# Kernel optimization log

Measured on AMD Instinct MI355X. Metric: run time of the kernel, lower is better.

## Reference

```python
import jax, jax.numpy as jnp
import numpy as np

B, H, W, C = 4, 64, 64, 256
D = C // 8  # reduction_ratio = 8


def setup_inputs() -> dict:
    key = jax.random.key(0)
    ks = jax.random.split(key, 6)
    scale = 1.0 / np.sqrt(C)
    return {
        "x": jax.random.normal(ks[0], (B, H, W, C), dtype=jnp.float32),
        "Wf": jax.random.normal(ks[1], (C, D), dtype=jnp.float32) * scale,
        "Wg": jax.random.normal(ks[2], (C, D), dtype=jnp.float32) * scale,
        "Wh": jax.random.normal(ks[3], (C, D), dtype=jnp.float32) * scale,
        "Wv": jax.random.normal(ks[4], (D, C), dtype=jnp.float32) * (1.0 / np.sqrt(D)),
        "gamma": jax.random.normal(ks[5], (), dtype=jnp.float32),
    }


def reference(x, Wf, Wg, Wh, Wv, gamma):
    b, h, w, c = x.shape
    n = h * w
    xf = x.reshape(b, n, c)
    # 1x1 convs (no bias) == per-pixel matmuls over channels
    q = xf @ Wf  # [b, n, d]
    k = xf @ Wg  # [b, n, d]
    v = xf @ Wh  # [b, n, d]
    # beta[i, j] = k_i . q_j ; softmax over last (query) axis, unscaled
    beta = jax.nn.softmax(jnp.einsum('bnd,bmd->bnm', k, q), axis=-1)  # [b, n, n]
    o = jnp.einsum('bnm,bmd->bnd', beta, v)  # [b, n, d]
    o = o.reshape(b, h, w, -1) @ Wv  # output 1x1 conv -> [b, h, w, c]
    return gamma * o + x
```

## Files before the change

kernel.cpp:

```cpp
#include <hip/hip_runtime.h>
#include <hip/hip_bf16.h>
#include <stdint.h>


typedef __attribute__((ext_vector_type(8))) short bf16x8;
typedef __attribute__((ext_vector_type(4))) float f32x4;
typedef unsigned short ushort_t;

static __device__ __forceinline__ ushort_t f2bf(float f) {
    __hip_bfloat16 h = __float2bfloat16(f);
    return __builtin_bit_cast(ushort_t, h);
}
static __device__ __forceinline__ float bf2f(ushort_t u) {
    return __bfloat162float(__builtin_bit_cast(__hip_bfloat16, u));
}

#define NROWS 16384
#define NTOK  4096
#define QKS   40
#define PVS   72

__global__ __launch_bounds__(256) void prep_kernel(
    const float* __restrict__ Wf, const float* __restrict__ Wg,
    const float* __restrict__ Wh,
    ushort_t* __restrict__ WhT, ushort_t* __restrict__ WlT,
    float* __restrict__ zero_base)
{
    int bid = blockIdx.x;
    if (bid < 96) {
        int id  = bid * 256 + threadIdx.x;
        int a   = id >> 13, rem = id & 8191;
        int k   = rem >> 5, d = rem & 31;
        const float* Wsrc = (a == 0) ? Wf : (a == 1) ? Wg : Wh;
        float val = Wsrc[rem];
        ushort_t hi = f2bf(val);
        WhT[(a * 32 + d) * 256 + k] = hi;
        WlT[(a * 32 + d) * 256 + k] = f2bf(val - bf2f(hi));
    } else {
        int i = (bid - 96) * 1024 + threadIdx.x * 4;
        *reinterpret_cast<float4*>(&zero_base[i]) = (float4){0.f, 0.f, 0.f, 0.f};
    }
}

__global__ __launch_bounds__(256) void qkv_kernel(
    const float* __restrict__ x,
    const ushort_t* __restrict__ WhT, const ushort_t* __restrict__ WlT,
    ushort_t* __restrict__ qh,
    ushort_t* __restrict__ kh, ushort_t* __restrict__ kl,
    ushort_t* __restrict__ vh)
{
    __shared__ __align__(16) ushort_t xh[64 * QKS];
    __shared__ __align__(16) ushort_t xl[64 * QKS];

    const int tid  = threadIdx.x;
    const int wave = tid >> 6;
    const int lane = tid & 63;
    const int ln15 = lane & 15;
    const int quad = lane >> 4;
    const int row0 = blockIdx.x * 64;
    const int r    = tid >> 2;
    const int pp   = (tid & 3) * 8;

    f32x4 acc[6];
    #pragma unroll
    for (int s = 0; s < 6; ++s) acc[s] = (f32x4){0.f, 0.f, 0.f, 0.f};

    float4 xa = *reinterpret_cast<const float4*>(&x[(row0 + r) * 256 + pp]);
    float4 xb = *reinterpret_cast<const float4*>(&x[(row0 + r) * 256 + pp + 4]);

    for (int k0 = 0; k0 < 256; k0 += 32) {
        bf16x8 bh[6], bl[6];
        #pragma unroll
        for (int s = 0; s < 6; ++s) {
            bh[s] = *reinterpret_cast<const bf16x8*>(
                &WhT[(s * 16 + ln15) * 256 + k0 + quad * 8]);
            bl[s] = *reinterpret_cast<const bf16x8*>(
                &WlT[(s * 16 + ln15) * 256 + k0 + quad * 8]);
        }
        float fv[8];
        *reinterpret_cast<float4*>(&fv[0]) = xa;
        *reinterpret_cast<float4*>(&fv[4]) = xb;
        ushort_t hv[8], lv[8];
        #pragma unroll
        for (int j = 0; j < 8; ++j) {
            hv[j] = f2bf(fv[j]);
            lv[j] = f2bf(fv[j] - bf2f(hv[j]));
        }
        __syncthreads();
        *reinterpret_cast<uint4*>(&xh[r * QKS + pp]) = *reinterpret_cast<uint4*>(hv);
        *reinterpret_cast<uint4*>(&xl[r * QKS + pp]) = *reinterpret_cast<uint4*>(lv);
        __syncthreads();
        if (k0 < 224) {
            xa = *reinterpret_cast<const float4*>(&x[(row0 + r) * 256 + k0 + 32 + pp]);
            xb = *reinterpret_cast<const float4*>(&x[(row0 + r) * 256 + k0 + 36 + pp]);
        }
        const bf16x8 ah = *reinterpret_cast<const bf16x8*>(
            &xh[(wave * 16 + ln15) * QKS + quad * 8]);
        const bf16x8 al = *reinterpret_cast<const bf16x8*>(
            &xl[(wave * 16 + ln15) * QKS + quad * 8]);
        #pragma unroll
        for (int s = 0; s < 6; ++s) {
            acc[s] = __builtin_amdgcn_mfma_f32_16x16x32_bf16(ah, bh[s], acc[s], 0, 0, 0);
            acc[s] = __builtin_amdgcn_mfma_f32_16x16x32_bf16(al, bh[s], acc[s], 0, 0, 0);
            acc[s] = __builtin_amdgcn_mfma_f32_16x16x32_bf16(ah, bl[s], acc[s], 0, 0, 0);
        }
    }

    #pragma unroll
    for (int s = 0; s < 6; ++s) {
        int cc = (s & 1) * 16 + ln15;
        #pragma unroll
        for (int rr = 0; rr < 4; ++rr) {
            int row = row0 + wave * 16 + quad * 4 + rr;
            float val = acc[s][rr];
            ushort_t hi = f2bf(val);
            if (s < 2) {
                qh[row * 32 + cc] = hi;
            } else if (s < 4) {
                kh[row * 32 + cc] = hi;
                kl[row * 32 + cc] = f2bf(val - bf2f(hi));
            } else {
                vh[row * 32 + cc] = hi;
            }
        }
    }
}

__global__ __launch_bounds__(256, 4) void attn_kernel(
    const ushort_t* __restrict__ qhg,
    const ushort_t* __restrict__ khg, const ushort_t* __restrict__ klg,
    const ushort_t* __restrict__ vhg,
    float* __restrict__ o_num, float* __restrict__ l_glob)
{
    __shared__ __align__(16) ushort_t Khs[64 * QKS];
    __shared__ __align__(16) ushort_t Kls[64 * QKS];
    __shared__ __align__(16) ushort_t Qhs[2][64 * QKS];
    __shared__ __align__(16) ushort_t Vth[2][32 * PVS];
    __shared__ __align__(16) ushort_t Ps[4 * 16 * PVS];

    const int tid  = threadIdx.x;
    const int wave = tid >> 6;
    const int lane = tid & 63;
    const int ln15 = lane & 15;
    const int quad = lane >> 4;

    const int rowtile = blockIdx.x & 255;
    const int chunk   = blockIdx.x >> 8;
    const int b    = rowtile >> 6;
    const int n0   = (rowtile & 63) * 64;
    const int base = b * NTOK;
    const int mt0  = chunk * 16;

    const int r = tid >> 2;
    const int p = (tid & 3) * 8;

    {
        uint4 a0 = *reinterpret_cast<const uint4*>(&khg[(base + n0 + r) * 32 + p]);
        *reinterpret_cast<uint4*>(&Khs[r * QKS + p]) = a0;
        uint4 a1 = *reinterpret_cast<const uint4*>(&klg[(base + n0 + r) * 32 + p]);
        *reinterpret_cast<uint4*>(&Kls[r * QKS + p]) = a1;
    }
    {
        int m0 = mt0 * 64;
        uint4 t0 = *reinterpret_cast<const uint4*>(&qhg[(base + m0 + r) * 32 + p]);
        *reinterpret_cast<uint4*>(&Qhs[0][r * QKS + p]) = t0;
        uint4 v0 = *reinterpret_cast<const uint4*>(&vhg[(base + m0 + r) * 32 + p]);
        const ushort_t* vs = reinterpret_cast<const ushort_t*>(&v0);
        #pragma unroll
        for (int j = 0; j < 8; ++j)
            Vth[0][(p + j) * PVS + r] = vs[j];
    }
    __syncthreads();

    const bf16x8 khf = *reinterpret_cast<const bf16x8*>(
        &Khs[(wave * 16 + ln15) * QKS + quad * 8]);
    const bf16x8 klf = *reinterpret_cast<const bf16x8*>(
        &Kls[(wave * 16 + ln15) * QKS + quad * 8]);

    f32x4 accO[2];
    accO[0] = (f32x4){0.f, 0.f, 0.f, 0.f};
    accO[1] = (f32x4){0.f, 0.f, 0.f, 0.f};
    float lacc[4] = {0.f, 0.f, 0.f, 0.f};

    int buf = 0;
    for (int it = 0; it < 16; ++it) {
        uint4 nqh, nvh;
        if (it < 15) {
            int m1 = (mt0 + it + 1) * 64;
            nqh = *reinterpret_cast<const uint4*>(&qhg[(base + m1 + r) * 32 + p]);
            nvh = *reinterpret_cast<const uint4*>(&vhg[(base + m1 + r) * 32 + p]);
        }

        f32x4 st[4];
        #pragma unroll
        for (int t = 0; t < 4; ++t) {
            const bf16x8 qf = *reinterpret_cast<const bf16x8*>(
                &Qhs[buf][(t * 16 + ln15) * QKS + quad * 8]);
            f32x4 s = __builtin_amdgcn_mfma_f32_16x16x32_bf16(
                khf, qf, (f32x4){0.f, 0.f, 0.f, 0.f}, 0, 0, 0);
            s = __builtin_amdgcn_mfma_f32_16x16x32_bf16(klf, qf, s, 0, 0, 0);
            st[t] = s;
        }

        #pragma unroll
        for (int t = 0; t < 4; ++t)
            #pragma unroll
            for (int rr = 0; rr < 4; ++rr)
                st[t][rr] = __expf(st[t][rr]);
        #pragma unroll
        for (int rr = 0; rr < 4; ++rr)
            lacc[rr] += st[0][rr] + st[1][rr] + st[2][rr] + st[3][rr];

        ushort_t* pw = &Ps[wave * 16 * PVS];
        #pragma unroll
        for (int t = 0; t < 4; ++t)
            #pragma unroll
            for (int rr = 0; rr < 4; ++rr)
                pw[(quad * 4 + rr) * PVS + t * 16 + ln15] = f2bf(st[t][rr]);

        #pragma unroll
        for (int kc = 0; kc < 2; ++kc) {
            const bf16x8 af = *reinterpret_cast<const bf16x8*>(
                &pw[ln15 * PVS + kc * 32 + quad * 8]);
            #pragma unroll
            for (int s01 = 0; s01 < 2; ++s01) {
                const bf16x8 bhf = *reinterpret_cast<const bf16x8*>(
                    &Vth[buf][(s01 * 16 + ln15) * PVS + kc * 32 + quad * 8]);
                accO[s01] = __builtin_amdgcn_mfma_f32_16x16x32_bf16(af, bhf, accO[s01], 0, 0, 0);
            }
        }

        if (it < 15) {
            *reinterpret_cast<uint4*>(&Qhs[buf ^ 1][r * QKS + p]) = nqh;
            const ushort_t* vs = reinterpret_cast<const ushort_t*>(&nvh);
            #pragma unroll
            for (int j = 0; j < 8; ++j)
                Vth[buf ^ 1][(p + j) * PVS + r] = vs[j];
            __syncthreads();
        }
        buf ^= 1;
    }

    #pragma unroll
    for (int rr = 0; rr < 4; ++rr) {
        float s0 = lacc[rr];
        #pragma unroll
        for (int off = 1; off < 16; off <<= 1)
            s0 += __shfl_xor(s0, off);
        lacc[rr] = s0;
    }
    const int row_base = base + n0 + wave * 16 + quad * 4;
    if (ln15 == 0) {
        #pragma unroll
        for (int rr = 0; rr < 4; ++rr)
            unsafeAtomicAdd(&l_glob[row_base + rr], lacc[rr]);
    }
    #pragma unroll
    for (int s01 = 0; s01 < 2; ++s01)
        #pragma unroll
        for (int rr = 0; rr < 4; ++rr)
            unsafeAtomicAdd(&o_num[(row_base + rr) * 32 + s01 * 16 + ln15],
                            accO[s01][rr]);
}

__global__ __launch_bounds__(256) void out_kernel(
    const float* __restrict__ o_num, const float* __restrict__ l_glob,
    const float* __restrict__ Wv, const float* __restrict__ x,
    const float* __restrict__ gamma, float* __restrict__ out)
{
    __shared__ float wv[8192];
    __shared__ float orow[32][32];
    __shared__ float linv[32];
    const int tid  = threadIdx.x;
    const int row0 = blockIdx.x * 32;

    for (int i = tid; i < 8192; i += 256) wv[i] = Wv[i];
    for (int i = tid; i < 1024; i += 256)
        orow[i >> 5][i & 31] = o_num[(row0 + (i >> 5)) * 32 + (i & 31)];
    if (tid < 32) linv[tid] = 1.0f / l_glob[row0 + tid];
    __syncthreads();

    const float g = gamma[0];
    #pragma unroll 4
    for (int rc = 0; rc < 32; rc += 8) {
        float acc[8];
        #pragma unroll
        for (int rr = 0; rr < 8; ++rr) acc[rr] = 0.f;
        for (int d = 0; d < 32; ++d) {
            float wvd = wv[d * 256 + tid];
            #pragma unroll
            for (int rr = 0; rr < 8; ++rr) acc[rr] += orow[rc + rr][d] * wvd;
        }
        #pragma unroll
        for (int rr = 0; rr < 8; ++rr) {
            int row = row0 + rc + rr;
            out[row * 256 + tid] = g * acc[rr] * linv[rc + rr] + x[row * 256 + tid];
        }
    }
}

extern "C" void kernel_launch(void* const* d_in, const int* in_sizes, int n_in,
                              void* d_out, int out_size, void* d_ws, size_t ws_size,
                              hipStream_t stream)
{
    const float* x     = (const float*)d_in[0];
    const float* Wf    = (const float*)d_in[1];
    const float* Wg    = (const float*)d_in[2];
    const float* Wh    = (const float*)d_in[3];
    const float* Wv    = (const float*)d_in[4];
    const float* gamma = (const float*)d_in[5];
    float* out = (float*)d_out;

    ushort_t* qh = (ushort_t*)d_ws;
    ushort_t* kh = qh + NROWS * 32;
    ushort_t* kl = kh + NROWS * 32;
    ushort_t* vh = kl + NROWS * 32;
    float* o_num  = (float*)(vh + NROWS * 32);
    float* l_glob = o_num + NROWS * 32;
    ushort_t* WhT = (ushort_t*)(l_glob + NROWS);
    ushort_t* WlT = WhT + 96 * 256;

    prep_kernel<<<dim3(624), dim3(256), 0, stream>>>(Wf, Wg, Wh, WhT, WlT, o_num);
    qkv_kernel<<<dim3(256), dim3(256), 0, stream>>>(x, WhT, WlT, qh, kh, kl, vh);
    attn_kernel<<<dim3(1024), dim3(256), 0, stream>>>(qh, kh, kl, vh, o_num, l_glob);
    out_kernel<<<dim3(512), dim3(256), 0, stream>>>(o_num, l_glob, Wv, x, gamma, out);
}
```

Measured before the change: 136.9 us.

## Drop prep kernel, store V transposed, and replace atomics with per-chunk partials

Removes the separate weight-prep and zeroing kernel by having qkv_kernel split the weights into bf16 hi/lo on the fly, and halves the qkv block size to double the grid. V is now written transposed in global memory, so attn_kernel loads it with vector stores instead of scattered LDS writes. The P tile in LDS gets an XOR swizzle to cut bank conflicts. Float atomics on o_num/l_glob become plain stores into four per-chunk partial buffers, which out_kernel sums, at the cost of extra workspace and reads.

```diff
diff --git a/kernel.cpp b/kernel.cpp
--- a/kernel.cpp
+++ b/kernel.cpp
@@ -19,109 +19,107 @@
 #define NTOK  4096
 #define QKS   40
 #define PVS   72
-
-__global__ __launch_bounds__(256) void prep_kernel(
+#define OPART (NROWS * 32)
+
+__global__ __launch_bounds__(256) void qkv_kernel(
+    const float* __restrict__ x,
     const float* __restrict__ Wf, const float* __restrict__ Wg,
     const float* __restrict__ Wh,
-    ushort_t* __restrict__ WhT, ushort_t* __restrict__ WlT,
-    float* __restrict__ zero_base)
-{
-    int bid = blockIdx.x;
-    if (bid < 96) {
-        int id  = bid * 256 + threadIdx.x;
-        int a   = id >> 13, rem = id & 8191;
-        int k   = rem >> 5, d = rem & 31;
-        const float* Wsrc = (a == 0) ? Wf : (a == 1) ? Wg : Wh;
-        float val = Wsrc[rem];
-        ushort_t hi = f2bf(val);
-        WhT[(a * 32 + d) * 256 + k] = hi;
-        WlT[(a * 32 + d) * 256 + k] = f2bf(val - bf2f(hi));
-    } else {
-        int i = (bid - 96) * 1024 + threadIdx.x * 4;
-        *reinterpret_cast<float4*>(&zero_base[i]) = (float4){0.f, 0.f, 0.f, 0.f};
-    }
-}
-
-__global__ __launch_bounds__(256) void qkv_kernel(
-    const float* __restrict__ x,
-    const ushort_t* __restrict__ WhT, const ushort_t* __restrict__ WlT,
     ushort_t* __restrict__ qh,
     ushort_t* __restrict__ kh, ushort_t* __restrict__ kl,
-    ushort_t* __restrict__ vh)
+    ushort_t* __restrict__ vT)
 {
-    __shared__ __align__(16) ushort_t xh[64 * QKS];
-    __shared__ __align__(16) ushort_t xl[64 * QKS];
+    __shared__ __align__(16) ushort_t xh[32 * QKS];
+    __shared__ __align__(16) ushort_t xl[32 * QKS];
 
     const int tid  = threadIdx.x;
     const int wave = tid >> 6;
     const int lane = tid & 63;
     const int ln15 = lane & 15;
     const int quad = lane >> 4;
-    const int row0 = blockIdx.x * 64;
-    const int r    = tid >> 2;
-    const int pp   = (tid & 3) * 8;
-
-    f32x4 acc[6];
+    const int row0 = blockIdx.x * 32;
+    const int rg     = wave & 1;
+    const int cgbase = wave >> 1;
+    const int r  = tid >> 3;
+    const int pp = (tid & 7) * 4;
+
+    f32x4 acc[3];
     #pragma unroll
-    for (int s = 0; s < 6; ++s) acc[s] = (f32x4){0.f, 0.f, 0.f, 0.f};
+    for (int ci = 0; ci < 3; ++ci) acc[ci] = (f32x4){0.f, 0.f, 0.f, 0.f};
 
     float4 xa = *reinterpret_cast<const float4*>(&x[(row0 + r) * 256 + pp]);
-    float4 xb = *reinterpret_cast<const float4*>(&x[(row0 + r) * 256 + pp + 4]);
 
     for (int k0 = 0; k0 < 256; k0 += 32) {
-        bf16x8 bh[6], bl[6];
-        #pragma unroll
-        for (int s = 0; s < 6; ++s) {
-            bh[s] = *reinterpret_cast<const bf16x8*>(
-                &WhT[(s * 16 + ln15) * 256 + k0 + quad * 8]);
-            bl[s] = *reinterpret_cast<const bf16x8*>(
-                &WlT[(s * 16 + ln15) * 256 + k0 + quad * 8]);
-        }
-        float fv[8];
-        *reinterpret_cast<float4*>(&fv[0]) = xa;
-        *reinterpret_cast<float4*>(&fv[4]) = xb;
-        ushort_t hv[8], lv[8];
-        #pragma unroll
-        for (int j = 0; j < 8; ++j) {
+        bf16x8 bh[3], bl[3];
+        #pragma unroll
+        for (int ci = 0; ci < 3; ++ci) {
+            int cg = cgbase + ci * 2;
+            const float* Wsrc = (cg < 2) ? Wf : (cg < 4) ? Wg : Wh;
+            int c = (cg & 1) * 16 + ln15;
+            ushort_t hv8[8], lv8[8];
+            #pragma unroll
+            for (int j = 0; j < 8; ++j) {
+                float w = Wsrc[(k0 + quad * 8 + j) * 32 + c];
+                ushort_t hi = f2bf(w);
+                hv8[j] = hi;
+                lv8[j] = f2bf(w - bf2f(hi));
+            }
+            bh[ci] = *reinterpret_cast<bf16x8*>(hv8);
+            bl[ci] = *reinterpret_cast<bf16x8*>(lv8);
+        }
+        float fv[4];
+        *reinterpret_cast<float4*>(fv) = xa;
+        ushort_t hv[4], lv[4];
+        #pragma unroll
+        for (int j = 0; j < 4; ++j) {
             hv[j] = f2bf(fv[j]);
             lv[j] = f2bf(fv[j] - bf2f(hv[j]));
         }
         __syncthreads();
-        *reinterpret_cast<uint4*>(&xh[r * QKS + pp]) = *reinterpret_cast<uint4*>(hv);
-        *reinterpret_cast<uint4*>(&xl[r * QKS + pp]) = *reinterpret_cast<uint4*>(lv);
+        *reinterpret_cast<uint2*>(&xh[r * QKS + pp]) = *reinterpret_cast<uint2*>(hv);
+        *reinterpret_cast<uint2*>(&xl[r * QKS + pp]) = *reinterpret_cast<uint2*>(lv);
         __syncthreads();
-        if (k0 < 224) {
+        if (k0 < 224)
             xa = *reinterpret_cast<const float4*>(&x[(row0 + r) * 256 + k0 + 32 + pp]);
-            xb = *reinterpret_cast<const float4*>(&x[(row0 + r) * 256 + k0 + 36 + pp]);
-        }
+
         const bf16x8 ah = *reinterpret_cast<const bf16x8*>(
-            &xh[(wave * 16 + ln15) * QKS + quad * 8]);
+            &xh[(rg * 16 + ln15) * QKS + quad * 8]);
         const bf16x8 al = *reinterpret_cast<const bf16x8*>(
-            &xl[(wave * 16 + ln15) * QKS + quad * 8]);
-        #pragma unroll
-        for (int s = 0; s < 6; ++s) {
-            acc[s] = __builtin_amdgcn_mfma_f32_16x16x32_bf16(ah, bh[s], acc[s], 0, 0, 0);
-            acc[s] = __builtin_amdgcn_mfma_f32_16x16x32_bf16(al, bh[s], acc[s], 0, 0, 0);
-            acc[s] = __builtin_amdgcn_mfma_f32_16x16x32_bf16(ah, bl[s], acc[s], 0, 0, 0);
+            &xl[(rg * 16 + ln15) * QKS + quad * 8]);
+        #pragma unroll
+        for (int ci = 0; ci < 3; ++ci) {
+            acc[ci] = __builtin_amdgcn_mfma_f32_16x16x32_bf16(ah, bh[ci], acc[ci], 0, 0, 0);
+            acc[ci] = __builtin_amdgcn_mfma_f32_16x16x32_bf16(al, bh[ci], acc[ci], 0, 0, 0);
+            acc[ci] = __builtin_amdgcn_mfma_f32_16x16x32_bf16(ah, bl[ci], acc[ci], 0, 0, 0);
         }
     }
 
     #pragma unroll
-    for (int s = 0; s < 6; ++s) {
-        int cc = (s & 1) * 16 + ln15;
-        #pragma unroll
-        for (int rr = 0; rr < 4; ++rr) {
-            int row = row0 + wave * 16 + quad * 4 + rr;
-            float val = acc[s][rr];
-            ushort_t hi = f2bf(val);
-            if (s < 2) {
-                qh[row * 32 + cc] = hi;
-            } else if (s < 4) {
-                kh[row * 32 + cc] = hi;
-                kl[row * 32 + cc] = f2bf(val - bf2f(hi));
-            } else {
-                vh[row * 32 + cc] = hi;
+    for (int ci = 0; ci < 3; ++ci) {
+        int cg = cgbase + ci * 2;
+        int cc = (cg & 1) * 16 + ln15;
+        int rowb = row0 + rg * 16 + quad * 4;
+        if (cg < 2) {
+            #pragma unroll
+            for (int rr = 0; rr < 4; ++rr)
+                qh[(rowb + rr) * 32 + cc] = f2bf(acc[ci][rr]);
+        } else if (cg < 4) {
+            #pragma unroll
+            for (int rr = 0; rr < 4; ++rr) {
+                float val = acc[ci][rr];
+                ushort_t hi = f2bf(val);
+                kh[(rowb + rr) * 32 + cc] = hi;
+                kl[(rowb + rr) * 32 + cc] = f2bf(val - bf2f(hi));
             }
+        } else {
+            int bb = row0 >> 12;
+            int m  = (row0 & 4095) + rg * 16 + quad * 4;
+            ushort4 h4;
+            h4.x = f2bf(acc[ci][0]);
+            h4.y = f2bf(acc[ci][1]);
+            h4.z = f2bf(acc[ci][2]);
+            h4.w = f2bf(acc[ci][3]);
+            *reinterpret_cast<ushort4*>(&vT[bb * 131072 + cc * 4096 + m]) = h4;
         }
     }
 }
@@ -129,8 +127,8 @@
 __global__ __launch_bounds__(256, 4) void attn_kernel(
     const ushort_t* __restrict__ qhg,
     const ushort_t* __restrict__ khg, const ushort_t* __restrict__ klg,
-    const ushort_t* __restrict__ vhg,
-    float* __restrict__ o_num, float* __restrict__ l_glob)
+    const ushort_t* __restrict__ vT,
+    float* __restrict__ o_part, float* __restrict__ l_part)
 {
     __shared__ __align__(16) ushort_t Khs[64 * QKS];
     __shared__ __align__(16) ushort_t Kls[64 * QKS];
@@ -149,10 +147,13 @@
     const int b    = rowtile >> 6;
     const int n0   = (rowtile & 63) * 64;
     const int base = b * NTOK;
+    const int bb   = b * 131072;
     const int mt0  = chunk * 16;
 
-    const int r = tid >> 2;
-    const int p = (tid & 3) * 8;
+    const int r  = tid >> 2;
+    const int p  = (tid & 3) * 8;
+    const int vd = tid >> 3;
+    const int vm = (tid & 7) * 8;
 
     {
         uint4 a0 = *reinterpret_cast<const uint4*>(&khg[(base + n0 + r) * 32 + p]);
@@ -164,11 +165,8 @@
         int m0 = mt0 * 64;
         uint4 t0 = *reinterpret_cast<const uint4*>(&qhg[(base + m0 + r) * 32 + p]);
         *reinterpret_cast<uint4*>(&Qhs[0][r * QKS + p]) = t0;
-        uint4 v0 = *reinterpret_cast<const uint4*>(&vhg[(base + m0 + r) * 32 + p]);
-        const ushort_t* vs = reinterpret_cast<const ushort_t*>(&v0);
-        #pragma unroll
-        for (int j = 0; j < 8; ++j)
-            Vth[0][(p + j) * PVS + r] = vs[j];
+        uint4 v0 = *reinterpret_cast<const uint4*>(&vT[bb + vd * 4096 + m0 + vm]);
+        *reinterpret_cast<uint4*>(&Vth[0][vd * PVS + vm]) = v0;
     }
     __syncthreads();
 
@@ -188,7 +186,7 @@
         if (it < 15) {
             int m1 = (mt0 + it + 1) * 64;
             nqh = *reinterpret_cast<const uint4*>(&qhg[(base + m1 + r) * 32 + p]);
-            nvh = *reinterpret_cast<const uint4*>(&vhg[(base + m1 + r) * 32 + p]);
+            nvh = *reinterpret_cast<const uint4*>(&vT[bb + vd * 4096 + m1 + vm]);
         }
 
         f32x4 st[4];
@@ -216,12 +214,13 @@
         for (int t = 0; t < 4; ++t)
             #pragma unroll
             for (int rr = 0; rr < 4; ++rr)
-                pw[(quad * 4 + rr) * PVS + t * 16 + ln15] = f2bf(st[t][rr]);
-
+                pw[(quad * 4 + rr) * PVS + ((t ^ quad) & 3) * 16 + ln15] = f2bf(st[t][rr]);
+
+        const int rq = (ln15 >> 2) & 3;
         #pragma unroll
         for (int kc = 0; kc < 2; ++kc) {
             const bf16x8 af = *reinterpret_cast<const bf16x8*>(
-                &pw[ln15 * PVS + kc * 32 + quad * 8]);
+                &pw[ln15 * PVS + (((kc * 32 + quad * 8) ^ (rq * 16)))]);
             #pragma unroll
             for (int s01 = 0; s01 < 2; ++s01) {
                 const bf16x8 bhf = *reinterpret_cast<const bf16x8*>(
@@ -232,10 +231,7 @@
 
         if (it < 15) {
             *reinterpret_cast<uint4*>(&Qhs[buf ^ 1][r * QKS + p]) = nqh;
-            const ushort_t* vs = reinterpret_cast<const ushort_t*>(&nvh);
-            #pragma unroll
-            for (int j = 0; j < 8; ++j)
-                Vth[buf ^ 1][(p + j) * PVS + r] = vs[j];
+            *reinterpret_cast<uint4*>(&Vth[buf ^ 1][vd * PVS + vm]) = nvh;
             __syncthreads();
         }
         buf ^= 1;
@@ -250,21 +246,21 @@
         lacc[rr] = s0;
     }
     const int row_base = base + n0 + wave * 16 + quad * 4;
+    float* op = o_part + (size_t)chunk * OPART;
     if (ln15 == 0) {
         #pragma unroll
         for (int rr = 0; rr < 4; ++rr)
-            unsafeAtomicAdd(&l_glob[row_base + rr], lacc[rr]);
+            l_part[chunk * NROWS + row_base + rr] = lacc[rr];
     }
     #pragma unroll
     for (int s01 = 0; s01 < 2; ++s01)
         #pragma unroll
         for (int rr = 0; rr < 4; ++rr)
-            unsafeAtomicAdd(&o_num[(row_base + rr) * 32 + s01 * 16 + ln15],
-                            accO[s01][rr]);
+            op[(row_base + rr) * 32 + s01 * 16 + ln15] = accO[s01][rr];
 }
 
 __global__ __launch_bounds__(256) void out_kernel(
-    const float* __restrict__ o_num, const float* __restrict__ l_glob,
+    const float* __restrict__ o_part, const float* __restrict__ l_part,
     const float* __restrict__ Wv, const float* __restrict__ x,
     const float* __restrict__ gamma, float* __restrict__ out)
 {
@@ -275,9 +271,17 @@
     const int row0 = blockIdx.x * 32;
 
     for (int i = tid; i < 8192; i += 256) wv[i] = Wv[i];
-    for (int i = tid; i < 1024; i += 256)
-        orow[i >> 5][i & 31] = o_num[(row0 + (i >> 5)) * 32 + (i & 31)];
-    if (tid < 32) linv[tid] = 1.0f / l_glob[row0 + tid];
+    for (int i = tid; i < 1024; i += 256) {
+        int rr = i >> 5, d = i & 31;
+        int idx = (row0 + rr) * 32 + d;
+        orow[rr][d] = o_part[idx] + o_part[OPART + idx]
+                    + o_part[2 * OPART + idx] + o_part[3 * OPART + idx];
+    }
+    if (tid < 32) {
+        int row = row0 + tid;
+        linv[tid] = 1.0f / (l_part[row] + l_part[NROWS + row]
+                          + l_part[2 * NROWS + row] + l_part[3 * NROWS + row]);
+    }
     __syncthreads();
 
     const float g = gamma[0];
@@ -314,14 +318,11 @@
     ushort_t* qh = (ushort_t*)d_ws;
     ushort_t* kh = qh + NROWS * 32;
     ushort_t* kl = kh + NROWS * 32;
-    ushort_t* vh = kl + NROWS * 32;
-    float* o_num  = (float*)(vh + NROWS * 32);
-    float* l_glob = o_num + NROWS * 32;
-    ushort_t* WhT = (ushort_t*)(l_glob + NROWS);
-    ushort_t* WlT = WhT + 96 * 256;
-
-    prep_kernel<<<dim3(624), dim3(256), 0, stream>>>(Wf, Wg, Wh, WhT, WlT, o_num);
-    qkv_kernel<<<dim3(256), dim3(256), 0, stream>>>(x, WhT, WlT, qh, kh, kl, vh);
-    attn_kernel<<<dim3(1024), dim3(256), 0, stream>>>(qh, kh, kl, vh, o_num, l_glob);
-    out_kernel<<<dim3(512), dim3(256), 0, stream>>>(o_num, l_glob, Wv, x, gamma, out);
-}
+    ushort_t* vT = kl + NROWS * 32;
+    float* o_part = (float*)(vT + NROWS * 32);
+    float* l_part = o_part + (size_t)4 * OPART;
+
+    qkv_kernel<<<dim3(512), dim3(256), 0, stream>>>(x, Wf, Wg, Wh, qh, kh, kl, vT);
+    attn_kernel<<<dim3(1024), dim3(256), 0, stream>>>(qh, kh, kl, vT, o_part, l_part);
+    out_kernel<<<dim3(512), dim3(256), 0, stream>>>(o_part, l_part, Wv, x, gamma, out);
+}
```

Result: faster. 125.2 us (-8.6%).
